# Performance work log

Measured on AMD Instinct MI355X. Metric: run time of the kernel, lower is better.

The kernel has to match this reference:

```python
import jax, jax.numpy as jnp
import numpy as np
import math

B, S, D = 16, 512, 512
H = 8
RET = 512  # return_dim, multiple of D
EPS = 1e-12


def _xavier(key, shape):
    bound = math.sqrt(6.0 / (shape[0] + shape[1]))
    return jax.random.uniform(key, shape, jnp.float32, -bound, bound)


def setup_inputs() -> dict:
    key = jax.random.key(0)
    ks = jax.random.split(key, 7)
    x = jax.random.normal(ks[0], (B, S, D), jnp.float32)
    WQ = _xavier(ks[1], (D, D))
    WK = _xavier(ks[2], (D, D))
    WV = _xavier(ks[3], (D, D))
    # LazyLinear over flattened (S*D) features; stored [in, out] for clean matmul
    Wlin = jax.random.normal(ks[4], (S * D, RET), jnp.float32) / math.sqrt(S * D)
    blin = jnp.zeros((RET,), jnp.float32)
    ln_w = jnp.ones((D,), jnp.float32)
    ln_b = jnp.zeros((D,), jnp.float32)
    return {"x": x, "WQ": WQ, "WK": WK, "WV": WV,
            "Wlin": Wlin, "blin": blin, "ln_w": ln_w, "ln_b": ln_b}


def _swish(v):
    return v * jax.nn.sigmoid(v)


def reference(x, WQ, WK, WV, Wlin, blin, ln_w, ln_b):
    b, s, d = x.shape
    dh = d // H
    # QKV projections -> [b, h, s, dh]
    Q = (x @ WQ).reshape(b, s, H, dh).transpose(0, 2, 1, 3)
    K = (x @ WK).reshape(b, s, H, dh).transpose(0, 2, 1, 3)
    V = (x @ WV).reshape(b, s, H, dh).transpose(0, 2, 1, 3)
    # swish-gated attention scores (no softmax)
    scores = jnp.einsum('bhqd,bhkd->bhqk', Q, K) / math.sqrt(dh)
    scores = _swish(scores)
    out = jnp.einsum('bhqk,bhkd->bqhd', scores, V).reshape(b, s, d)
    # residual + TF-style LayerNorm (residual_coef = 1)
    out = out + x
    u = out.mean(-1, keepdims=True)
    var = jnp.mean((out - u) ** 2, axis=-1, keepdims=True)
    out = ln_w * ((out - u) / jnp.sqrt(var + EPS)) + ln_b
    # linear over flattened seq*d features, swish, reshape (dropout = identity, eval)
    y = out.reshape(b, -1) @ Wlin + blin
    y = _swish(y)
    return y.reshape(b, -1, d)
```

## Files before the change

kernel.cpp:

```cpp
#include <hip/hip_runtime.h>
#include <cstdint>

#define TB 16
#define TS 512
#define TD 512
#define TH 8
#define TDH 64
#define TSD (TS*TD)

typedef __attribute__((ext_vector_type(8))) short s16x8;
typedef __attribute__((ext_vector_type(4))) float f32x4;
typedef unsigned short bfu;

__device__ __forceinline__ unsigned cvt_pk(float lo, float hi) {
  unsigned r;
  asm("v_cvt_pk_bf16_f32 %0, %1, %2" : "=v"(r) : "v"(lo), "v"(hi));
  return r;
}
__device__ __forceinline__ unsigned short f2b(float f) {
  unsigned r;
  asm("v_cvt_pk_bf16_f32 %0, %1, %2" : "=v"(r) : "v"(f), "v"(f));
  return (unsigned short)r;
}
__device__ __forceinline__ float b2f(bfu h) {
  return __uint_as_float(((unsigned)h) << 16);
}

__device__ __forceinline__ void gll16(const void* g, void* l) {
  __builtin_amdgcn_global_load_lds((const __attribute__((address_space(1))) void*)g,
                                   (__attribute__((address_space(3))) void*)l, 16, 0, 0);
}

__device__ __forceinline__ f32x4 MFMA16(s16x8 a, s16x8 b, f32x4 c) {
  return __builtin_amdgcn_mfma_f32_16x16x32_bf16(a, b, c, 0, 0, 0);
}

__global__ __launch_bounds__(256) void k_prep(const float* __restrict__ x, uint2* __restrict__ xb,
                                              const float* __restrict__ WQ, const float* __restrict__ WK,
                                              const float* __restrict__ WV, bfu* __restrict__ wt) {
  int t = threadIdx.x;
  if (blockIdx.x < 4096) {
    int i = blockIdx.x * 256 + t;
    float4 v = ((const float4*)x)[i];
    uint2 o; o.x = cvt_pk(v.x, v.y); o.y = cvt_pk(v.z, v.w);
    xb[i] = o;
    return;
  }
  __shared__ float tile[64][65];
  int bid = blockIdx.x - 4096;
  int bk = bid & 7;
  int bn = bid >> 3;
  const float* W = bn < 8 ? WQ : (bn < 16 ? WK : WV);
  int ncol0 = (bn & 7) * 64;
  int tx = t & 63, ty = t >> 6;
  #pragma unroll
  for (int i = 0; i < 16; ++i) {
    int kl = i * 4 + ty;
    tile[kl][tx] = W[(size_t)(bk * 64 + kl) * 512 + ncol0 + tx];
  }
  __syncthreads();
  #pragma unroll
  for (int i = 0; i < 16; ++i) {
    int nl = i * 4 + ty;
    wt[(size_t)(bn * 64 + nl) * 512 + bk * 64 + tx] = f2b(tile[tx][nl]);
  }
}

__global__ __launch_bounds__(256) void k_qkv(const bfu* __restrict__ xb, const bfu* __restrict__ wt,
                                             bfu* __restrict__ qb, bfu* __restrict__ kb, bfu* __restrict__ vtb) {
  __shared__ __align__(16) bfu At[2][128 * 32];
  __shared__ __align__(16) bfu Bt[2][128 * 32];
  int t = threadIdx.x, lane = t & 63, w = t >> 6;
  int wr = w >> 1, wc = w & 1;
  int m0 = blockIdx.x * 128, n0 = blockIdx.y * 128;
  int fr = lane & 15, hi = lane >> 4;
  int l4r = lane >> 2, l4c = lane & 3;
  f32x4 acc[4][4] = {};

#define QKV_STAGE(BUF, K0) { \
    _Pragma("unroll") \
    for (int i = 0; i < 2; ++i) { \
      int row = i * 64 + w * 16 + l4r; \
      int cs = l4c ^ (l4r & 3); \
      gll16(xb + (size_t)(m0 + row) * TD + (K0) + cs * 8, (char*)At[BUF] + (i * 256 + w * 64) * 16); \
      gll16(wt + (size_t)(n0 + row) * TD + (K0) + cs * 8, (char*)Bt[BUF] + (i * 256 + w * 64) * 16); \
    } }

#define QKV_COMP(BUF) { \
    s16x8 a[4], bb[4]; \
    int ca = (hi ^ (fr & 3)) * 8; \
    _Pragma("unroll") \
    for (int m = 0; m < 4; ++m) a[m]  = *(const s16x8*)&At[BUF][(wr * 64 + m * 16 + fr) * 32 + ca]; \
    _Pragma("unroll") \
    for (int n = 0; n < 4; ++n) bb[n] = *(const s16x8*)&Bt[BUF][(wc * 64 + n * 16 + fr) * 32 + ca]; \
    _Pragma("unroll") \
    for (int m = 0; m < 4; ++m) \
      _Pragma("unroll") \
      for (int n = 0; n < 4; ++n) \
        acc[m][n] = MFMA16(a[m], bb[n], acc[m][n]); }

  QKV_STAGE(0, 0)
  __syncthreads();
  for (int k = 0; k < 16; ++k) {
    int cur = k & 1;
    if (k < 15) QKV_STAGE(cur ^ 1, (k + 1) * 32)
    QKV_COMP(cur)
    __syncthreads();
  }
#undef QKV_STAGE
#undef QKV_COMP

  #pragma unroll
  for (int m = 0; m < 4; ++m) {
    int grow = m0 + wr * 64 + m * 16 + hi * 4;
    #pragma unroll
    for (int n = 0; n < 4; ++n) {
      int gcol = n0 + wc * 64 + n * 16 + fr;
      if (gcol < 512) {
        #pragma unroll
        for (int r = 0; r < 4; ++r) qb[(size_t)(grow + r) * TD + gcol] = f2b(acc[m][n][r]);
      } else if (gcol < 1024) {
        int c = gcol - 512;
        #pragma unroll
        for (int r = 0; r < 4; ++r) kb[(size_t)(grow + r) * TD + c] = f2b(acc[m][n][r]);
      } else {
        int c = gcol - 1024;
        int hh = c >> 6, dc = c & 63;
        int b_ = grow >> 9, s = grow & 511;
        ushort4 pk;
        pk.x = f2b(acc[m][n][0]); pk.y = f2b(acc[m][n][1]);
        pk.z = f2b(acc[m][n][2]); pk.w = f2b(acc[m][n][3]);
        *(ushort4*)&vtb[((size_t)((b_ * TH + hh) * TDH + dc) << 9) + s] = pk;
      }
    }
  }
}

__global__ __launch_bounds__(256) void k_attn(const bfu* __restrict__ qb, const bfu* __restrict__ kb,
                                              const bfu* __restrict__ vtb, const bfu* __restrict__ xb,
                                              float* __restrict__ ao) {
  __shared__ __align__(16) bfu Qs[64 * 64];
  __shared__ __align__(16) bfu Ks[128 * 64];
  __shared__ __align__(16) bfu Vs[64 * 128];
  __shared__ __align__(16) bfu Ps[64 * 128];
  int t = threadIdx.x, lane = t & 63, w = t >> 6;
  int qt = blockIdx.x, h = blockIdx.y, b = blockIdx.z;
  size_t qrow0 = (size_t)b * TS + qt * 64;
  int fr = lane & 15, hi = lane >> 4;
  int l8r = lane >> 3, l8c = lane & 7;
  int l16r = lane >> 4, l16c = lane & 15;

#define K_STAGE(KT) { \
    _Pragma("unroll") \
    for (int i = 0; i < 4; ++i) { \
      int row = i * 32 + w * 8 + l8r; \
      int cs = l8c ^ (l8r & 7); \
      gll16(kb + ((size_t)b * TS + (KT) * 128 + row) * TD + h * TDH + cs * 8, \
            (char*)Ks + (i * 256 + w * 64) * 16); \
    } }
#define V_STAGE(KT) { \
    _Pragma("unroll") \
    for (int i = 0; i < 4; ++i) { \
      int row = i * 16 + w * 4 + l16r; \
      int cs = l16c ^ (row & 7); \
      gll16(vtb + ((size_t)(b * TH + h) * TDH + row) * TS + (KT) * 128 + cs * 8, \
            (char*)Vs + (i * 256 + w * 64) * 16); \
    } }

  #pragma unroll
  for (int i = 0; i < 2; ++i) {
    int row = i * 32 + w * 8 + l8r;
    int cs = l8c ^ (l8r & 7);
    gll16(qb + (qrow0 + row) * TD + h * TDH + cs * 8, (char*)Qs + (i * 256 + w * 64) * 16);
  }
  K_STAGE(0)
  V_STAGE(0)
  __syncthreads();

  int qrow = w * 16 + fr;
  int r7 = fr & 7;
  f32x4 acc_o[4] = {};
  for (int kt = 0; kt < 4; ++kt) {
    s16x8 aq0 = *(const s16x8*)&Qs[qrow * 64 + ((hi ^ r7) * 8)];
    s16x8 aq1 = *(const s16x8*)&Qs[qrow * 64 + (((4 + hi) ^ r7) * 8)];
    f32x4 sc[8];
    #pragma unroll
    for (int kj = 0; kj < 8; ++kj) {
      int krow = kj * 16 + fr;
      s16x8 b0 = *(const s16x8*)&Ks[krow * 64 + ((hi ^ r7) * 8)];
      s16x8 b1 = *(const s16x8*)&Ks[krow * 64 + (((4 + hi) ^ r7) * 8)];
      f32x4 c = {};
      c = MFMA16(aq0, b0, c);
      c = MFMA16(aq1, b1, c);
      sc[kj] = c;
    }
    #pragma unroll
    for (int kj = 0; kj < 8; ++kj) {
      #pragma unroll
      for (int r = 0; r < 4; ++r) {
        float v = sc[kj][r] * 0.125f;
        float p = v / (1.f + __expf(-v));
        int prow = w * 16 + hi * 4 + r;
        int c8 = (kj * 2 + (fr >> 3)) ^ (prow & 7);
        Ps[prow * 128 + c8 * 8 + (fr & 7)] = f2b(p);
      }
    }
    #pragma unroll
    for (int ks = 0; ks < 4; ++ks) {
      s16x8 pa = *(const s16x8*)&Ps[qrow * 128 + (((ks * 4 + hi) ^ r7) * 8)];
      #pragma unroll
      for (int dn = 0; dn < 4; ++dn) {
        s16x8 vb = *(const s16x8*)&Vs[(dn * 16 + fr) * 128 + (((ks * 4 + hi) ^ r7) * 8)];
        acc_o[dn] = MFMA16(pa, vb, acc_o[dn]);
      }
    }
    __syncthreads();
    if (kt < 3) {
      K_STAGE(kt + 1)
      V_STAGE(kt + 1)
      __syncthreads();
    }
  }
#undef K_STAGE
#undef V_STAGE
  #pragma unroll
  for (int dn = 0; dn < 4; ++dn) {
    int col = h * TDH + dn * 16 + fr;
    #pragma unroll
    for (int r = 0; r < 4; ++r) {
      size_t row = qrow0 + w * 16 + hi * 4 + r;
      ao[row * TD + col] = acc_o[dn][r] + b2f(xb[row * TD + col]);
    }
  }
}

__global__ __launch_bounds__(256) void k_ln(const float* __restrict__ a, const float* __restrict__ w,
                                            const float* __restrict__ bias, bfu* __restrict__ o) {
  int row = blockIdx.x, t = threadIdx.x;
  float2 v = *(const float2*)(a + (size_t)row * TD + t * 2);
  float s = v.x + v.y;
  #pragma unroll
  for (int off = 32; off > 0; off >>= 1) s += __shfl_down(s, off);
  __shared__ float r1[4], r2[4];
  int lane = t & 63, wv = t >> 6;
  if (lane == 0) r1[wv] = s;
  __syncthreads();
  float mean = (r1[0] + r1[1] + r1[2] + r1[3]) * (1.f / TD);
  float dx = v.x - mean, dy = v.y - mean;
  float q = dx * dx + dy * dy;
  #pragma unroll
  for (int off = 32; off > 0; off >>= 1) q += __shfl_down(q, off);
  if (lane == 0) r2[wv] = q;
  __syncthreads();
  float var = (r2[0] + r2[1] + r2[2] + r2[3]) * (1.f / TD);
  float inv = rsqrtf(var + 1e-12f);
  float2 wv2 = *(const float2*)(w + t * 2);
  float2 bv2 = *(const float2*)(bias + t * 2);
  unsigned pack = cvt_pk(wv2.x * dx * inv + bv2.x, wv2.y * dy * inv + bv2.y);
  *(unsigned*)(o + (size_t)row * TD + t * 2) = pack;
}

__global__ __launch_bounds__(256) void k_lin_mfma(const bfu* __restrict__ lno, const float* __restrict__ wl,
                                                  float* __restrict__ part) {
  __shared__ __align__(16) bfu Wt[2][64 * 72];
  int t = threadIdx.x, lane = t & 63, w = t >> 6;
  int fr = lane & 15, hi = lane >> 4;
  int kc = blockIdx.x >> 3, nb = blockIdx.x & 7;
  int n0 = nb * 64;
  int nl = t & 63, kb = (t >> 6) * 16;
  int ks0 = kc * 2048;
  const float* wbase = wl + (size_t)(ks0 + kb) * 512 + n0 + nl;
  const bfu*   abase = lno + (size_t)fr * TSD + ks0 + hi * 8;
  f32x4 acc = {};
  float wreg[16];
  #pragma unroll
  for (int i = 0; i < 16; ++i) wreg[i] = __builtin_nontemporal_load(wbase + (size_t)i * 512);
  for (int s = 0; s < 32; ++s) {
    int cur = s & 1;
    unsigned pk[8];
    #pragma unroll
    for (int i = 0; i < 8; ++i) pk[i] = cvt_pk(wreg[2 * i], wreg[2 * i + 1]);
    *(uint4*)&Wt[cur][nl * 72 + kb]     = *(uint4*)&pk[0];
    *(uint4*)&Wt[cur][nl * 72 + kb + 8] = *(uint4*)&pk[4];
    if (s < 31) {
      const float* wp2 = wbase + (size_t)(s + 1) * 64 * 512;
      #pragma unroll
      for (int i = 0; i < 16; ++i) wreg[i] = __builtin_nontemporal_load(wp2 + (size_t)i * 512);
    }
    s16x8 a0 = *(const s16x8*)(abase + s * 64);
    s16x8 a1 = *(const s16x8*)(abase + s * 64 + 32);
    __syncthreads();
    s16x8 b0 = *(const s16x8*)&Wt[cur][(w * 16 + fr) * 72 + hi * 8];
    s16x8 b1 = *(const s16x8*)&Wt[cur][(w * 16 + fr) * 72 + 32 + hi * 8];
    acc = MFMA16(a0, b0, acc);
    acc = MFMA16(a1, b1, acc);
  }
  #pragma unroll
  for (int r = 0; r < 4; ++r)
    part[(size_t)kc * 8192 + (hi * 4 + r) * 512 + n0 + w * 16 + fr] = acc[r];
}

__global__ __launch_bounds__(256) void k_lin_red(const float* __restrict__ part, const float* __restrict__ blin,
                                                 float* __restrict__ out) {
  int o = blockIdx.x * 256 + threadIdx.x;
  float s = 0.f;
  #pragma unroll 16
  for (int c = 0; c < 128; ++c) s += part[(size_t)c * 8192 + o];
  float v = s + blin[o & 511];
  out[o] = v / (1.f + __expf(-v));
}

extern "C" void kernel_launch(void* const* d_in, const int* in_sizes, int n_in,
                              void* d_out, int out_size, void* d_ws, size_t ws_size,
                              hipStream_t stream) {
  const float* x   = (const float*)d_in[0];
  const float* WQ  = (const float*)d_in[1];
  const float* WK  = (const float*)d_in[2];
  const float* WV  = (const float*)d_in[3];
  const float* Wl  = (const float*)d_in[4];
  const float* bl  = (const float*)d_in[5];
  const float* lnw = (const float*)d_in[6];
  const float* lnb = (const float*)d_in[7];
  float* out = (float*)d_out;
  char* ws = (char*)d_ws;
  bfu* xb  = (bfu*)ws;
  bfu* wt  = xb + 4194304;
  bfu* qb  = wt + 786432;
  bfu* kb  = qb + 4194304;
  bfu* vtb = kb + 4194304;
  float* attn = (float*)(vtb + 4194304);
  bfu*   lno  = (bfu*)(attn + 4194304);
  float* part = (float*)(lno + 4194304);

  k_prep    <<<4288, 256, 0, stream>>>(x, (uint2*)xb, WQ, WK, WV, wt);
  k_qkv     <<<dim3(64, 12), 256, 0, stream>>>(xb, wt, qb, kb, vtb);
  k_attn    <<<dim3(8, 8, 16), 256, 0, stream>>>(qb, kb, vtb, xb, attn);
  k_ln      <<<8192, 256, 0, stream>>>(attn, lnw, lnb, lno);
  k_lin_mfma<<<1024, 256, 0, stream>>>(lno, Wl, part);
  k_lin_red <<<32, 256, 0, stream>>>(part, bl, out);
}
```

Measured before the change: 184.5 us.

## Fuse attention, LayerNorm and flattened linear into one ticketed persistent-style kernel

Attention, LayerNorm and the split-K linear are merged into one launch. Blocks take atomic tickets: the first 1024 do attention and write per-head row sum and sum-of-squares partials, and the rest compute the linear. Linear blocks prefetch their weights, spin on per-query-tile completion counters, then apply LayerNorm on the fly from the fp32 attention output. The goal is to remove the separate LN kernel, its bf16 round trip and launch gaps, and to overlap streaming the big weight matrix with attention compute. The cost is spin-waiting, a single-pass variance formula, an extra memset, and Q fragments now read straight from global memory instead of LDS.

```diff
diff --git a/kernel.cpp b/kernel.cpp
--- a/kernel.cpp
+++ b/kernel.cpp
@@ -136,19 +136,29 @@
   }
 }
 
-__global__ __launch_bounds__(256) void k_attn(const bfu* __restrict__ qb, const bfu* __restrict__ kb,
-                                              const bfu* __restrict__ vtb, const bfu* __restrict__ xb,
-                                              float* __restrict__ ao) {
-  __shared__ __align__(16) bfu Qs[64 * 64];
-  __shared__ __align__(16) bfu Ks[128 * 64];
-  __shared__ __align__(16) bfu Vs[64 * 128];
-  __shared__ __align__(16) bfu Ps[64 * 128];
+__global__ __launch_bounds__(256) void k_fused(const bfu* __restrict__ qb, const bfu* __restrict__ kb,
+                                               const bfu* __restrict__ vtb, const bfu* __restrict__ xb,
+                                               const float* __restrict__ wl, const float* __restrict__ lnw,
+                                               const float* __restrict__ lnb, float* __restrict__ ao,
+                                               float* __restrict__ sp, float* __restrict__ part,
+                                               unsigned* flags) {
+  __shared__ __align__(16) char smem[49152];
+  __shared__ unsigned tkt_s;
   int t = threadIdx.x, lane = t & 63, w = t >> 6;
-  int qt = blockIdx.x, h = blockIdx.y, b = blockIdx.z;
-  size_t qrow0 = (size_t)b * TS + qt * 64;
   int fr = lane & 15, hi = lane >> 4;
-  int l8r = lane >> 3, l8c = lane & 7;
-  int l16r = lane >> 4, l16c = lane & 15;
+  if (t == 0) tkt_s = atomicAdd(&flags[0], 1u);
+  __syncthreads();
+  unsigned tk = tkt_s;
+  unsigned* done = flags + 1;
+
+  if (tk < 1024) {
+    int qt = tk >> 7, h = (tk >> 4) & 7, b = tk & 15;
+    bfu* Ks = (bfu*)smem;
+    bfu* Vs = (bfu*)(smem + 16384);
+    bfu* Ps = (bfu*)(smem + 32768);
+    size_t qrow0 = (size_t)b * TS + qt * 64;
+    int l8r = lane >> 3, l8c = lane & 7;
+    int l16r = lane >> 4, l16c = lane & 15;
 
 #define K_STAGE(KT) { \
     _Pragma("unroll") \
@@ -167,137 +177,164 @@
             (char*)Vs + (i * 256 + w * 64) * 16); \
     } }
 
-  #pragma unroll
-  for (int i = 0; i < 2; ++i) {
-    int row = i * 32 + w * 8 + l8r;
-    int cs = l8c ^ (l8r & 7);
-    gll16(qb + (qrow0 + row) * TD + h * TDH + cs * 8, (char*)Qs + (i * 256 + w * 64) * 16);
-  }
-  K_STAGE(0)
-  V_STAGE(0)
-  __syncthreads();
-
-  int qrow = w * 16 + fr;
-  int r7 = fr & 7;
-  f32x4 acc_o[4] = {};
-  for (int kt = 0; kt < 4; ++kt) {
-    s16x8 aq0 = *(const s16x8*)&Qs[qrow * 64 + ((hi ^ r7) * 8)];
-    s16x8 aq1 = *(const s16x8*)&Qs[qrow * 64 + (((4 + hi) ^ r7) * 8)];
-    f32x4 sc[8];
-    #pragma unroll
-    for (int kj = 0; kj < 8; ++kj) {
-      int krow = kj * 16 + fr;
-      s16x8 b0 = *(const s16x8*)&Ks[krow * 64 + ((hi ^ r7) * 8)];
-      s16x8 b1 = *(const s16x8*)&Ks[krow * 64 + (((4 + hi) ^ r7) * 8)];
-      f32x4 c = {};
-      c = MFMA16(aq0, b0, c);
-      c = MFMA16(aq1, b1, c);
-      sc[kj] = c;
-    }
-    #pragma unroll
-    for (int kj = 0; kj < 8; ++kj) {
-      #pragma unroll
-      for (int r = 0; r < 4; ++r) {
-        float v = sc[kj][r] * 0.125f;
-        float p = v / (1.f + __expf(-v));
-        int prow = w * 16 + hi * 4 + r;
-        int c8 = (kj * 2 + (fr >> 3)) ^ (prow & 7);
-        Ps[prow * 128 + c8 * 8 + (fr & 7)] = f2b(p);
-      }
-    }
-    #pragma unroll
-    for (int ks = 0; ks < 4; ++ks) {
-      s16x8 pa = *(const s16x8*)&Ps[qrow * 128 + (((ks * 4 + hi) ^ r7) * 8)];
-      #pragma unroll
-      for (int dn = 0; dn < 4; ++dn) {
-        s16x8 vb = *(const s16x8*)&Vs[(dn * 16 + fr) * 128 + (((ks * 4 + hi) ^ r7) * 8)];
-        acc_o[dn] = MFMA16(pa, vb, acc_o[dn]);
-      }
-    }
+    int qrow = w * 16 + fr;
+    const bfu* qp = qb + (qrow0 + qrow) * TD + h * TDH;
+    s16x8 aq0 = *(const s16x8*)(qp + hi * 8);
+    s16x8 aq1 = *(const s16x8*)(qp + 32 + hi * 8);
+
+    K_STAGE(0)
+    V_STAGE(0)
     __syncthreads();
-    if (kt < 3) {
-      K_STAGE(kt + 1)
-      V_STAGE(kt + 1)
+
+    int r7 = fr & 7;
+    f32x4 acc_o[4] = {};
+    for (int kt = 0; kt < 4; ++kt) {
+      f32x4 sc[8];
+      #pragma unroll
+      for (int kj = 0; kj < 8; ++kj) {
+        int krow = kj * 16 + fr;
+        s16x8 b0 = *(const s16x8*)&Ks[krow * 64 + ((hi ^ r7) * 8)];
+        s16x8 b1 = *(const s16x8*)&Ks[krow * 64 + (((4 + hi) ^ r7) * 8)];
+        f32x4 c = {};
+        c = MFMA16(aq0, b0, c);
+        c = MFMA16(aq1, b1, c);
+        sc[kj] = c;
+      }
+      #pragma unroll
+      for (int kj = 0; kj < 8; ++kj) {
+        #pragma unroll
+        for (int r = 0; r < 4; ++r) {
+          float v = sc[kj][r] * 0.125f;
+          float p = v / (1.f + __expf(-v));
+          int prow = w * 16 + hi * 4 + r;
+          int c8 = (kj * 2 + (fr >> 3)) ^ (prow & 7);
+          Ps[prow * 128 + c8 * 8 + (fr & 7)] = f2b(p);
+        }
+      }
+      #pragma unroll
+      for (int ks = 0; ks < 4; ++ks) {
+        s16x8 pa = *(const s16x8*)&Ps[qrow * 128 + (((ks * 4 + hi) ^ r7) * 8)];
+        #pragma unroll
+        for (int dn = 0; dn < 4; ++dn) {
+          s16x8 vb = *(const s16x8*)&Vs[(dn * 16 + fr) * 128 + (((ks * 4 + hi) ^ r7) * 8)];
+          acc_o[dn] = MFMA16(pa, vb, acc_o[dn]);
+        }
+      }
       __syncthreads();
-    }
-  }
+      if (kt < 3) {
+        K_STAGE(kt + 1)
+        V_STAGE(kt + 1)
+        __syncthreads();
+      }
+    }
 #undef K_STAGE
 #undef V_STAGE
-  #pragma unroll
-  for (int dn = 0; dn < 4; ++dn) {
-    int col = h * TDH + dn * 16 + fr;
+    float ps[4] = {0.f, 0.f, 0.f, 0.f}, ps2[4] = {0.f, 0.f, 0.f, 0.f};
+    #pragma unroll
+    for (int dn = 0; dn < 4; ++dn) {
+      int col = h * TDH + dn * 16 + fr;
+      #pragma unroll
+      for (int r = 0; r < 4; ++r) {
+        size_t row = qrow0 + w * 16 + hi * 4 + r;
+        float val = acc_o[dn][r] + b2f(xb[row * TD + col]);
+        ao[row * TD + col] = val;
+        ps[r] += val; ps2[r] += val * val;
+      }
+    }
     #pragma unroll
     for (int r = 0; r < 4; ++r) {
-      size_t row = qrow0 + w * 16 + hi * 4 + r;
-      ao[row * TD + col] = acc_o[dn][r] + b2f(xb[row * TD + col]);
-    }
-  }
-}
-
-__global__ __launch_bounds__(256) void k_ln(const float* __restrict__ a, const float* __restrict__ w,
-                                            const float* __restrict__ bias, bfu* __restrict__ o) {
-  int row = blockIdx.x, t = threadIdx.x;
-  float2 v = *(const float2*)(a + (size_t)row * TD + t * 2);
-  float s = v.x + v.y;
-  #pragma unroll
-  for (int off = 32; off > 0; off >>= 1) s += __shfl_down(s, off);
-  __shared__ float r1[4], r2[4];
-  int lane = t & 63, wv = t >> 6;
-  if (lane == 0) r1[wv] = s;
-  __syncthreads();
-  float mean = (r1[0] + r1[1] + r1[2] + r1[3]) * (1.f / TD);
-  float dx = v.x - mean, dy = v.y - mean;
-  float q = dx * dx + dy * dy;
-  #pragma unroll
-  for (int off = 32; off > 0; off >>= 1) q += __shfl_down(q, off);
-  if (lane == 0) r2[wv] = q;
-  __syncthreads();
-  float var = (r2[0] + r2[1] + r2[2] + r2[3]) * (1.f / TD);
-  float inv = rsqrtf(var + 1e-12f);
-  float2 wv2 = *(const float2*)(w + t * 2);
-  float2 bv2 = *(const float2*)(bias + t * 2);
-  unsigned pack = cvt_pk(wv2.x * dx * inv + bv2.x, wv2.y * dy * inv + bv2.y);
-  *(unsigned*)(o + (size_t)row * TD + t * 2) = pack;
-}
-
-__global__ __launch_bounds__(256) void k_lin_mfma(const bfu* __restrict__ lno, const float* __restrict__ wl,
-                                                  float* __restrict__ part) {
-  __shared__ __align__(16) bfu Wt[2][64 * 72];
-  int t = threadIdx.x, lane = t & 63, w = t >> 6;
-  int fr = lane & 15, hi = lane >> 4;
-  int kc = blockIdx.x >> 3, nb = blockIdx.x & 7;
-  int n0 = nb * 64;
-  int nl = t & 63, kb = (t >> 6) * 16;
-  int ks0 = kc * 2048;
-  const float* wbase = wl + (size_t)(ks0 + kb) * 512 + n0 + nl;
-  const bfu*   abase = lno + (size_t)fr * TSD + ks0 + hi * 8;
-  f32x4 acc = {};
-  float wreg[16];
-  #pragma unroll
-  for (int i = 0; i < 16; ++i) wreg[i] = __builtin_nontemporal_load(wbase + (size_t)i * 512);
-  for (int s = 0; s < 32; ++s) {
-    int cur = s & 1;
-    unsigned pk[8];
-    #pragma unroll
-    for (int i = 0; i < 8; ++i) pk[i] = cvt_pk(wreg[2 * i], wreg[2 * i + 1]);
-    *(uint4*)&Wt[cur][nl * 72 + kb]     = *(uint4*)&pk[0];
-    *(uint4*)&Wt[cur][nl * 72 + kb + 8] = *(uint4*)&pk[4];
-    if (s < 31) {
-      const float* wp2 = wbase + (size_t)(s + 1) * 64 * 512;
-      #pragma unroll
-      for (int i = 0; i < 16; ++i) wreg[i] = __builtin_nontemporal_load(wp2 + (size_t)i * 512);
-    }
-    s16x8 a0 = *(const s16x8*)(abase + s * 64);
-    s16x8 a1 = *(const s16x8*)(abase + s * 64 + 32);
+      float a = ps[r], q = ps2[r];
+      #pragma unroll
+      for (int off = 1; off < 16; off <<= 1) {
+        a += __shfl_xor(a, off, 16);
+        q += __shfl_xor(q, off, 16);
+      }
+      if (fr == 0) {
+        int row = (int)(qrow0 + w * 16 + hi * 4 + r);
+        sp[(size_t)row * 16 + h * 2]     = a;
+        sp[(size_t)row * 16 + h * 2 + 1] = q;
+      }
+    }
     __syncthreads();
-    s16x8 b0 = *(const s16x8*)&Wt[cur][(w * 16 + fr) * 72 + hi * 8];
-    s16x8 b1 = *(const s16x8*)&Wt[cur][(w * 16 + fr) * 72 + 32 + hi * 8];
-    acc = MFMA16(a0, b0, acc);
-    acc = MFMA16(a1, b1, acc);
-  }
-  #pragma unroll
-  for (int r = 0; r < 4; ++r)
-    part[(size_t)kc * 8192 + (hi * 4 + r) * 512 + n0 + w * 16 + fr] = acc[r];
+    if (t == 0) {
+      __threadfence();
+      __hip_atomic_fetch_add(&done[qt], 1u, __ATOMIC_RELEASE, __HIP_MEMORY_SCOPE_AGENT);
+    }
+  } else {
+    int c = (int)tk - 1024;
+    int kc = c >> 3, nb = c & 7;
+    int qtn = kc >> 4;
+    bfu*   Wt   = (bfu*)smem;
+    float* lg   = (float*)(smem + 18432);
+    float* lb   = (float*)(smem + 20480);
+    float* mu_s = (float*)(smem + 22528);
+    float* iv_s = (float*)(smem + 22784);
+    lg[t] = lnw[t]; lg[t + 256] = lnw[t + 256];
+    lb[t] = lnb[t]; lb[t + 256] = lnb[t + 256];
+    int n0 = nb * 64;
+    int nl = t & 63, kbo = (t >> 6) * 16;
+    const float* wbase = wl + (size_t)(kc * 2048 + kbo) * 512 + n0 + nl;
+    float wreg[16];
+    #pragma unroll
+    for (int i = 0; i < 16; ++i) wreg[i] = __builtin_nontemporal_load(wbase + (size_t)i * 512);
+    while (__hip_atomic_load(&done[qtn], __ATOMIC_ACQUIRE, __HIP_MEMORY_SCOPE_AGENT) < 128u)
+      __builtin_amdgcn_s_sleep(8);
+    if (t < 64) {
+      int bb = t & 15, sl = t >> 4;
+      int row = bb * 512 + 4 * kc + sl;
+      float s1 = 0.f, s2 = 0.f;
+      #pragma unroll
+      for (int hh = 0; hh < 8; ++hh) {
+        s1 += sp[(size_t)row * 16 + hh * 2];
+        s2 += sp[(size_t)row * 16 + hh * 2 + 1];
+      }
+      float mu = s1 * (1.f / 512.f);
+      float var = s2 * (1.f / 512.f) - mu * mu;
+      mu_s[sl * 16 + bb] = mu;
+      iv_s[sl * 16 + bb] = rsqrtf(var + 1e-12f);
+    }
+    __syncthreads();
+    f32x4 acc = {};
+    for (int s = 0; s < 32; ++s) {
+      int cur = s & 1;
+      unsigned pk[8];
+      #pragma unroll
+      for (int i = 0; i < 8; ++i) pk[i] = cvt_pk(wreg[2 * i], wreg[2 * i + 1]);
+      *(uint4*)&Wt[cur * 4608 + nl * 72 + kbo]     = *(uint4*)&pk[0];
+      *(uint4*)&Wt[cur * 4608 + nl * 72 + kbo + 8] = *(uint4*)&pk[4];
+      if (s < 31) {
+        const float* wp2 = wbase + (size_t)(s + 1) * 64 * 512;
+        #pragma unroll
+        for (int i = 0; i < 16; ++i) wreg[i] = __builtin_nontemporal_load(wp2 + (size_t)i * 512);
+      }
+      int sl = s >> 3, d0 = (s & 7) * 64;
+      const float* zp = ao + ((size_t)fr * 512 + (4 * kc + sl)) * 512 + d0 + hi * 8;
+      float4 za = *(const float4*)zp,        zbv = *(const float4*)(zp + 4);
+      float4 zc = *(const float4*)(zp + 32), zd  = *(const float4*)(zp + 36);
+      float mu = mu_s[sl * 16 + fr], iv = iv_s[sl * 16 + fr];
+      const float4 g0 = *(const float4*)&lg[d0 + hi * 8],      g1 = *(const float4*)&lg[d0 + hi * 8 + 4];
+      const float4 g2 = *(const float4*)&lg[d0 + 32 + hi * 8], g3 = *(const float4*)&lg[d0 + 32 + hi * 8 + 4];
+      const float4 b0v = *(const float4*)&lb[d0 + hi * 8],      b1v = *(const float4*)&lb[d0 + hi * 8 + 4];
+      const float4 b2v = *(const float4*)&lb[d0 + 32 + hi * 8], b3v = *(const float4*)&lb[d0 + 32 + hi * 8 + 4];
+      union { unsigned u[4]; s16x8 v; } a0u, a1u;
+      a0u.u[0] = cvt_pk(fmaf((za.x - mu) * iv, g0.x, b0v.x), fmaf((za.y - mu) * iv, g0.y, b0v.y));
+      a0u.u[1] = cvt_pk(fmaf((za.z - mu) * iv, g0.z, b0v.z), fmaf((za.w - mu) * iv, g0.w, b0v.w));
+      a0u.u[2] = cvt_pk(fmaf((zbv.x - mu) * iv, g1.x, b1v.x), fmaf((zbv.y - mu) * iv, g1.y, b1v.y));
+      a0u.u[3] = cvt_pk(fmaf((zbv.z - mu) * iv, g1.z, b1v.z), fmaf((zbv.w - mu) * iv, g1.w, b1v.w));
+      a1u.u[0] = cvt_pk(fmaf((zc.x - mu) * iv, g2.x, b2v.x), fmaf((zc.y - mu) * iv, g2.y, b2v.y));
+      a1u.u[1] = cvt_pk(fmaf((zc.z - mu) * iv, g2.z, b2v.z), fmaf((zc.w - mu) * iv, g2.w, b2v.w));
+      a1u.u[2] = cvt_pk(fmaf((zd.x - mu) * iv, g3.x, b3v.x), fmaf((zd.y - mu) * iv, g3.y, b3v.y));
+      a1u.u[3] = cvt_pk(fmaf((zd.z - mu) * iv, g3.z, b3v.z), fmaf((zd.w - mu) * iv, g3.w, b3v.w));
+      __syncthreads();
+      s16x8 bb0 = *(const s16x8*)&Wt[cur * 4608 + (w * 16 + fr) * 72 + hi * 8];
+      s16x8 bb1 = *(const s16x8*)&Wt[cur * 4608 + (w * 16 + fr) * 72 + 32 + hi * 8];
+      acc = MFMA16(a0u.v, bb0, acc);
+      acc = MFMA16(a1u.v, bb1, acc);
+    }
+    #pragma unroll
+    for (int r = 0; r < 4; ++r)
+      part[(size_t)kc * 8192 + (hi * 4 + r) * 512 + n0 + w * 16 + fr] = acc[r];
+  }
 }
 
 __global__ __launch_bounds__(256) void k_lin_red(const float* __restrict__ part, const float* __restrict__ blin,
@@ -328,14 +365,14 @@
   bfu* qb  = wt + 786432;
   bfu* kb  = qb + 4194304;
   bfu* vtb = kb + 4194304;
-  float* attn = (float*)(vtb + 4194304);
-  bfu*   lno  = (bfu*)(attn + 4194304);
-  float* part = (float*)(lno + 4194304);
-
-  k_prep    <<<4288, 256, 0, stream>>>(x, (uint2*)xb, WQ, WK, WV, wt);
-  k_qkv     <<<dim3(64, 12), 256, 0, stream>>>(xb, wt, qb, kb, vtb);
-  k_attn    <<<dim3(8, 8, 16), 256, 0, stream>>>(qb, kb, vtb, xb, attn);
-  k_ln      <<<8192, 256, 0, stream>>>(attn, lnw, lnb, lno);
-  k_lin_mfma<<<1024, 256, 0, stream>>>(lno, Wl, part);
-  k_lin_red <<<32, 256, 0, stream>>>(part, bl, out);
-}
+  float* attn  = (float*)(vtb + 4194304);
+  float* part  = attn + 4194304;
+  float* sp    = part + 1048576;
+  unsigned* flags = (unsigned*)(sp + 131072);
+
+  hipMemsetAsync(flags, 0, 16 * sizeof(unsigned), stream);
+  k_prep   <<<4288, 256, 0, stream>>>(x, (uint2*)xb, WQ, WK, WV, wt);
+  k_qkv    <<<dim3(64, 12), 256, 0, stream>>>(xb, wt, qb, kb, vtb);
+  k_fused  <<<2048, 256, 0, stream>>>(qb, kb, vtb, xb, Wl, lnw, lnb, attn, sp, part, flags);
+  k_lin_red<<<32, 256, 0, stream>>>(part, bl, out);
+}
```

After: 315.7 us. 71.1% more time.

## Prefetch Wlin into last-level cache via extra blocks in QKV and attention kernels

Applied to the files above, without the earlier changes.

Extra blocks are appended to the QKV and attention grids, with both grids flattened to 1D. The extra blocks stream about 160MB of the large fp32 Wlin matrix and write dummy sums, so that part of the later linear layer's weight traffic overlaps with compute-bound kernels and may be served from the infinity cache. The final split-K reduction is also split into two stages with more blocks, to increase parallelism over the 128 partials. The risks are that the prefetched lines get evicted before k_lin_mfma runs, and that the extra blocks take CU time and bandwidth from the attention and QKV work. LDS arrays in k_attn are padded, which increases LDS use.

```diff
diff --git a/kernel.cpp b/kernel.cpp
--- a/kernel.cpp
+++ b/kernel.cpp
@@ -67,12 +67,26 @@
 }
 
 __global__ __launch_bounds__(256) void k_qkv(const bfu* __restrict__ xb, const bfu* __restrict__ wt,
-                                             bfu* __restrict__ qb, bfu* __restrict__ kb, bfu* __restrict__ vtb) {
+                                             bfu* __restrict__ qb, bfu* __restrict__ kb, bfu* __restrict__ vtb,
+                                             const float* __restrict__ wl, float* __restrict__ dummy) {
+  int t = threadIdx.x;
+  if (blockIdx.x >= 768) {
+    int pb = blockIdx.x - 768;
+    const float4* wp = (const float4*)wl + (size_t)pb * 16384 + t;
+    float4 s4 = {0.f, 0.f, 0.f, 0.f};
+    #pragma unroll 8
+    for (int i = 0; i < 64; ++i) {
+      float4 v = wp[(size_t)i * 256];
+      s4.x += v.x; s4.y += v.y; s4.z += v.z; s4.w += v.w;
+    }
+    dummy[pb * 256 + t] = s4.x + s4.y + s4.z + s4.w;
+    return;
+  }
   __shared__ __align__(16) bfu At[2][128 * 32];
   __shared__ __align__(16) bfu Bt[2][128 * 32];
-  int t = threadIdx.x, lane = t & 63, w = t >> 6;
+  int lane = t & 63, w = t >> 6;
   int wr = w >> 1, wc = w & 1;
-  int m0 = blockIdx.x * 128, n0 = blockIdx.y * 128;
+  int m0 = (blockIdx.x & 63) * 128, n0 = (blockIdx.x >> 6) * 128;
   int fr = lane & 15, hi = lane >> 4;
   int l4r = lane >> 2, l4c = lane & 3;
   f32x4 acc[4][4] = {};
@@ -138,18 +152,40 @@
 
 __global__ __launch_bounds__(256) void k_attn(const bfu* __restrict__ qb, const bfu* __restrict__ kb,
                                               const bfu* __restrict__ vtb, const bfu* __restrict__ xb,
-                                              float* __restrict__ ao) {
-  __shared__ __align__(16) bfu Qs[64 * 64];
-  __shared__ __align__(16) bfu Ks[128 * 64];
-  __shared__ __align__(16) bfu Vs[64 * 128];
-  __shared__ __align__(16) bfu Ps[64 * 128];
-  int t = threadIdx.x, lane = t & 63, w = t >> 6;
-  int qt = blockIdx.x, h = blockIdx.y, b = blockIdx.z;
+                                              float* __restrict__ ao,
+                                              const float* __restrict__ wl, float* __restrict__ dummy) {
+  int t = threadIdx.x;
+  if (blockIdx.x >= 1024) {
+    int pb = blockIdx.x - 1024;
+    const float4* wp = (const float4*)wl + 4194304 + (size_t)pb * 16384 + t;
+    float4 s4 = {0.f, 0.f, 0.f, 0.f};
+    #pragma unroll 8
+    for (int i = 0; i < 64; ++i) {
+      float4 v = wp[(size_t)i * 256];
+      s4.x += v.x; s4.y += v.y; s4.z += v.z; s4.w += v.w;
+    }
+    dummy[(256 + pb) * 256 + t] = s4.x + s4.y + s4.z + s4.w;
+    return;
+  }
+  __shared__ __align__(16) bfu Qs[64 * 72];
+  __shared__ __align__(16) bfu Ks[128 * 72];
+  __shared__ __align__(16) bfu Vs[64 * 136];
+  __shared__ __align__(16) bfu Ps[64 * 136];
+  int lane = t & 63, w = t >> 6;
+  int qt = blockIdx.x & 7, h = (blockIdx.x >> 3) & 7, b = blockIdx.x >> 6;
   size_t qrow0 = (size_t)b * TS + qt * 64;
   int fr = lane & 15, hi = lane >> 4;
   int l8r = lane >> 3, l8c = lane & 7;
   int l16r = lane >> 4, l16c = lane & 15;
 
+  {
+    #pragma unroll
+    for (int i = 0; i < 2; ++i) {
+      int row = i * 32 + w * 8 + l8r;
+      int cs = l8c ^ (l8r & 7);
+      gll16(qb + (qrow0 + row) * TD + h * TDH + cs * 8, (char*)Qs + (i * 256 + w * 64) * 16);
+    }
+  }
 #define K_STAGE(KT) { \
     _Pragma("unroll") \
     for (int i = 0; i < 4; ++i) { \
@@ -166,13 +202,6 @@
       gll16(vtb + ((size_t)(b * TH + h) * TDH + row) * TS + (KT) * 128 + cs * 8, \
             (char*)Vs + (i * 256 + w * 64) * 16); \
     } }
-
-  #pragma unroll
-  for (int i = 0; i < 2; ++i) {
-    int row = i * 32 + w * 8 + l8r;
-    int cs = l8c ^ (l8r & 7);
-    gll16(qb + (qrow0 + row) * TD + h * TDH + cs * 8, (char*)Qs + (i * 256 + w * 64) * 16);
-  }
   K_STAGE(0)
   V_STAGE(0)
   __syncthreads();
@@ -300,12 +329,23 @@
     part[(size_t)kc * 8192 + (hi * 4 + r) * 512 + n0 + w * 16 + fr] = acc[r];
 }
 
-__global__ __launch_bounds__(256) void k_lin_red(const float* __restrict__ part, const float* __restrict__ blin,
-                                                 float* __restrict__ out) {
+__global__ __launch_bounds__(256) void k_lin_red1(const float* __restrict__ part, float* __restrict__ part2) {
+  int t = threadIdx.x;
+  int cs = blockIdx.x >> 5;
+  int ob = blockIdx.x & 31;
+  int o = ob * 256 + t;
+  float s = 0.f;
+  #pragma unroll 16
+  for (int c = cs * 16; c < cs * 16 + 16; ++c) s += part[(size_t)c * 8192 + o];
+  part2[(size_t)cs * 8192 + o] = s;
+}
+
+__global__ __launch_bounds__(256) void k_lin_red2(const float* __restrict__ part2, const float* __restrict__ blin,
+                                                  float* __restrict__ out) {
   int o = blockIdx.x * 256 + threadIdx.x;
   float s = 0.f;
-  #pragma unroll 16
-  for (int c = 0; c < 128; ++c) s += part[(size_t)c * 8192 + o];
+  #pragma unroll
+  for (int c = 0; c < 8; ++c) s += part2[(size_t)c * 8192 + o];
   float v = s + blin[o & 511];
   out[o] = v / (1.f + __expf(-v));
 }
@@ -328,14 +368,17 @@
   bfu* qb  = wt + 786432;
   bfu* kb  = qb + 4194304;
   bfu* vtb = kb + 4194304;
-  float* attn = (float*)(vtb + 4194304);
-  bfu*   lno  = (bfu*)(attn + 4194304);
-  float* part = (float*)(lno + 4194304);
+  float* attn  = (float*)(vtb + 4194304);
+  bfu*   lno   = (bfu*)(attn + 4194304);
+  float* part  = (float*)(lno + 4194304);
+  float* part2 = part + 1048576;
+  float* dummy = part2 + 65536;
 
   k_prep    <<<4288, 256, 0, stream>>>(x, (uint2*)xb, WQ, WK, WV, wt);
-  k_qkv     <<<dim3(64, 12), 256, 0, stream>>>(xb, wt, qb, kb, vtb);
-  k_attn    <<<dim3(8, 8, 16), 256, 0, stream>>>(qb, kb, vtb, xb, attn);
+  k_qkv     <<<1024, 256, 0, stream>>>(xb, wt, qb, kb, vtb, Wl, dummy);
+  k_attn    <<<1408, 256, 0, stream>>>(qb, kb, vtb, xb, attn, Wl, dummy);
   k_ln      <<<8192, 256, 0, stream>>>(attn, lnw, lnb, lno);
   k_lin_mfma<<<1024, 256, 0, stream>>>(lno, Wl, part);
-  k_lin_red <<<32, 256, 0, stream>>>(part, bl, out);
-}
+  k_lin_red1<<<256, 256, 0, stream>>>(part, part2);
+  k_lin_red2<<<32, 256, 0, stream>>>(part2, bl, out);
+}
```

Measured after the change: 204.7 us. 1.11x slower.
